# Optimization experiments

Measured on AMD Instinct MI355X. Metric: run time of the kernel, lower is better.

Reference implementation:

```python
import jax, jax.numpy as jnp
import numpy as np

N, E, B, H = 20000, 100000, 512, 64
IN_CH, EDGE_DIM, OUT_CH = 16, 8, 1


def setup_inputs() -> dict:
    key = jax.random.key(0)
    ks = jax.random.split(key, 20)
    rn = lambda k, shp, s=0.1: (jax.random.normal(k, shp, jnp.float32) * s)
    return {
        'x': rn(ks[0], (N, IN_CH), 1.0),
        'edge_index': jax.random.randint(ks[1], (2, E), 0, N),
        'edge_attr': rn(ks[2], (E, EDGE_DIM), 1.0),
        'batch': jnp.sort(jax.random.randint(ks[3], (N,), 0, B)),
        'lin0_w': rn(ks[4], (IN_CH, H)), 'lin0_b': jnp.zeros((H,), jnp.float32),
        'nn1_w': rn(ks[5], (EDGE_DIM, 128)), 'nn1_b': jnp.zeros((128,), jnp.float32),
        'nn2_w': rn(ks[6], (128, H * H), 0.02), 'nn2_b': jnp.zeros((H * H,), jnp.float32),
        'root_w': rn(ks[7], (H, H)), 'root_b': jnp.zeros((H,), jnp.float32),
        'gru_wih': rn(ks[8], (H, 3 * H)), 'gru_whh': rn(ks[9], (H, 3 * H)),
        'gru_bih': jnp.zeros((3 * H,), jnp.float32), 'gru_bhh': jnp.zeros((3 * H,), jnp.float32),
        'lstm_wih': rn(ks[10], (2 * H, 4 * H)), 'lstm_whh': rn(ks[11], (H, 4 * H)),
        'lstm_bih': jnp.zeros((4 * H,), jnp.float32), 'lstm_bhh': jnp.zeros((4 * H,), jnp.float32),
        'lin1_w': rn(ks[12], (2 * H, H)), 'lin1_b': jnp.zeros((H,), jnp.float32),
        'lin2_w': rn(ks[13], (H, OUT_CH)), 'lin2_b': jnp.zeros((OUT_CH,), jnp.float32),
    }


def reference(x, edge_index, edge_attr, batch, lin0_w, lin0_b, nn1_w, nn1_b,
              nn2_w, nn2_b, root_w, root_b, gru_wih, gru_whh, gru_bih, gru_bhh,
              lstm_wih, lstm_whh, lstm_bih, lstm_bhh, lin1_w, lin1_b, lin2_w, lin2_b):
    src, dst = edge_index[0], edge_index[1]
    # edge network weights (shared across the 3 message-passing steps)
    ew = jax.nn.relu(edge_attr @ nn1_w + nn1_b) @ nn2_w + nn2_b  # [E, H*H]
    ew = ew.reshape(E, H, H)
    deg = jnp.maximum(jax.ops.segment_sum(jnp.ones((E,), x.dtype), dst, N), 1.0)

    out = jax.nn.relu(x @ lin0_w + lin0_b)  # [N, H]
    h = out
    for _ in range(3):
        # NNConv: gather src feats, per-edge matvec, scatter-mean to dst, + root linear
        msg = jnp.einsum('ei,eio->eo', out[src], ew)                  # [E, H]
        agg = jax.ops.segment_sum(msg, dst, N) / deg[:, None]          # [N, H]
        m = jax.nn.relu(agg + out @ root_w + root_b)
        # GRU cell (torch gate order r, z, n)
        gi = m @ gru_wih + gru_bih
        gh = h @ gru_whh + gru_bhh
        r = jax.nn.sigmoid(gi[:, :H] + gh[:, :H])
        z = jax.nn.sigmoid(gi[:, H:2 * H] + gh[:, H:2 * H])
        n = jnp.tanh(gi[:, 2 * H:] + r * gh[:, 2 * H:])
        h = (1.0 - z) * n + z * h
        out = h

    # Set2Set pooling, 3 processing steps (torch LSTM gate order i, f, g, o)
    q_star = jnp.zeros((B, 2 * H), x.dtype)
    hh = jnp.zeros((B, H), x.dtype)
    cc = jnp.zeros((B, H), x.dtype)
    for _ in range(3):
        g = q_star @ lstm_wih + hh @ lstm_whh + lstm_bih + lstm_bhh    # [B, 4H]
        i_g = jax.nn.sigmoid(g[:, :H])
        f_g = jax.nn.sigmoid(g[:, H:2 * H])
        g_g = jnp.tanh(g[:, 2 * H:3 * H])
        o_g = jax.nn.sigmoid(g[:, 3 * H:])
        cc = f_g * cc + i_g * g_g
        hh = o_g * jnp.tanh(cc)
        q = hh                                                          # [B, H]
        e = jnp.sum(out * q[batch], axis=-1)                            # [N]
        e_max = jax.ops.segment_max(e, batch, B)
        a = jnp.exp(e - e_max[batch])
        a = a / jax.ops.segment_sum(a, batch, B)[batch]
        rvec = jax.ops.segment_sum(a[:, None] * out, batch, B)          # [B, H]
        q_star = jnp.concatenate([q, rvec], axis=-1)

    y = jax.nn.relu(q_star @ lin1_w + lin1_b) @ lin2_w + lin2_b         # [B, 1]
    return y
```

## Files before the change

### kernel.cpp

```cpp
#include <hip/hip_runtime.h>
#include <hip/hip_bf16.h>
#include <hip/hip_fp16.h>
#include <cstddef>
#include <cstdint>

#define N_NODES 20000
#define N_EDGES 100000
#define N_BATCH 512

typedef __attribute__((ext_vector_type(8))) short ushort8_t;
typedef __attribute__((ext_vector_type(8))) _Float16 f16x8;
typedef __attribute__((ext_vector_type(4))) float f32x4;

union F16x8U { f16x8 v; unsigned int u[4]; };

__device__ __forceinline__ float sigmoidf_(float x) { return 1.f / (1.f + expf(-x)); }
__device__ __forceinline__ unsigned short f2h(float x) {
    return __half_as_ushort(__float2half(x));
}

#define HB_BLOCKS 50000
#define LIN0_BLOCKS 5000
#define BSW_BLOCKS 258
#define DEG_BLOCKS 391

__global__ __launch_bounds__(256) void prep_kernel(
        const float* __restrict__ ea, const float* __restrict__ w1, const float* __restrict__ b1,
        const float* __restrict__ x, const float* __restrict__ l0w, const float* __restrict__ l0b,
        const float* __restrict__ w2, const float* __restrict__ b2,
        const int* __restrict__ ei,
        unsigned short* __restrict__ hb, float* __restrict__ out,
        unsigned short* __restrict__ bsw, float* __restrict__ deg, int E) {
    int bid = blockIdx.x, tid = threadIdx.x;
    if (bid < HB_BLOCKS) {
        int idx = bid * 256 + tid;
        int e = idx >> 7, j = idx & 127;
        float acc = b1[j];
#pragma unroll
        for (int i = 0; i < 8; i++) acc += ea[e * 8 + i] * w1[i * 128 + j];
        hb[idx] = f2h(fmaxf(acc, 0.f));
    } else if (bid < HB_BLOCKS + LIN0_BLOCKS) {
        int idx = (bid - HB_BLOCKS) * 256 + tid;
        int n = idx >> 6, j = idx & 63;
        float acc = l0b[j];
#pragma unroll
        for (int i = 0; i < 16; i++) acc += x[n * 16 + i] * l0w[i * 64 + j];
        out[idx] = fmaxf(acc, 0.f);
    } else if (bid < HB_BLOCKS + LIN0_BLOCKS + BSW_BLOCKS) {
        int idx = (bid - HB_BLOCKS - LIN0_BLOCKS) * 256 + tid;
        if (idx < 66048) {
            int l = idx & 63, oc = (idx >> 6) & 3, ks = idx >> 8;
            int o = oc * 16 + (l & 15);
            int kap0 = ks * 32 + 8 * (l >> 4);
#pragma unroll
            for (int j = 0; j < 8; ++j) {
                int kap = kap0 + j;
                int k = kap >> 6, i = kap & 63;
                float v = (k < 128) ? w2[(size_t)k * 4096 + i * 64 + o] : b2[i * 64 + o];
                bsw[(size_t)idx * 8 + j] = f2h(v);
            }
        }
    } else {
        int e = (bid - HB_BLOCKS - LIN0_BLOCKS - BSW_BLOCKS) * 256 + tid;
        if (e < E) atomicAdd(&deg[ei[E + e]], 1.0f);
    }
}

__global__ __launch_bounds__(256) void msg_mfma(const float* __restrict__ out,
                                                const unsigned short* __restrict__ hb,
                                                const unsigned short* __restrict__ bsw,
                                                const int* __restrict__ ei,
                                                float* __restrict__ agg, int E) {
    __shared__ __align__(16) unsigned int hs[129 * 64];
    const int tid = threadIdx.x;
    const int w = tid >> 6, l = tid & 63;
    const int e0 = blockIdx.x * 64;
    const int r16 = l & 15, q = l >> 4;

    {
        int e = e0 + l;
        bool v = e < E;
        const ushort8_t* hrow = (const ushort8_t*)(hb + (size_t)e * 128);
#pragma unroll
        for (int cc = 0; cc < 4; ++cc) {
            int c = w * 4 + cc;
            ushort8_t hv = {};
            if (v) hv = hrow[c];
#pragma unroll
            for (int j = 0; j < 8; ++j) {
                unsigned int hu = (unsigned short)hv[j];
                hs[(c * 8 + j) * 64 + l] = (hu << 16) | hu;
            }
        }
        if (w == 0) hs[128 * 64 + l] = v ? 0x3C003C00u : 0u;
    }

    f16x8 sfrag[4][2];
#pragma unroll
    for (int t = 0; t < 4; ++t) {
        int e = e0 + t * 16 + r16;
        int src = (e < E) ? ei[e] : 0;
        const f32x4* p = (const f32x4*)(out + (size_t)src * 64);
#pragma unroll
        for (int st = 0; st < 2; ++st) {
            f16x8 f = {};
            if (e < E) {
                f32x4 a = p[st * 8 + q * 2], b = p[st * 8 + q * 2 + 1];
#pragma unroll
                for (int j = 0; j < 4; ++j) { f[j] = (_Float16)a[j]; f[4 + j] = (_Float16)b[j]; }
            }
            sfrag[t][st] = f;
        }
    }

    const f16x8* bp = (const f16x8*)bsw;
    f16x8 bfA[8], bfB[8];
#pragma unroll
    for (int i = 0; i < 8; ++i) bfA[i] = bp[((w * 8 + i) << 6) + l];

    __syncthreads();

    f32x4 acc[4][4] = {};

#define MSG_COMPUTE(K, BF)                                                     \
    {                                                                          \
        _Pragma("unroll")                                                      \
        for (int t = 0; t < 4; ++t) {                                          \
            unsigned int hh = hs[(K) * 64 + t * 16 + r16];                     \
            _Pragma("unroll")                                                  \
            for (int st = 0; st < 2; ++st) {                                   \
                F16x8U s_, a_;                                                 \
                s_.v = sfrag[t][st];                                           \
                asm("v_pk_mul_f16 %0, %1, %2" : "=v"(a_.u[0]) : "v"(hh), "v"(s_.u[0])); \
                asm("v_pk_mul_f16 %0, %1, %2" : "=v"(a_.u[1]) : "v"(hh), "v"(s_.u[1])); \
                asm("v_pk_mul_f16 %0, %1, %2" : "=v"(a_.u[2]) : "v"(hh), "v"(s_.u[2])); \
                asm("v_pk_mul_f16 %0, %1, %2" : "=v"(a_.u[3]) : "v"(hh), "v"(s_.u[3])); \
                _Pragma("unroll")                                              \
                for (int oc = 0; oc < 4; ++oc)                                 \
                    acc[t][oc] = __builtin_amdgcn_mfma_f32_16x16x32_f16(       \
                        a_.v, BF[st * 4 + oc], acc[t][oc], 0, 0, 0);           \
            }                                                                  \
        }                                                                      \
    }

#pragma unroll 1
    for (int kk = 0; kk < 16; ++kk) {
        int k1 = w + kk * 8;
        int k2 = k1 + 4;
#pragma unroll
        for (int i = 0; i < 8; ++i) bfB[i] = bp[((k2 * 8 + i) << 6) + l];
        MSG_COMPUTE(k1, bfA);
        if (kk < 15) {
            int k3 = k1 + 8;
#pragma unroll
            for (int i = 0; i < 8; ++i) bfA[i] = bp[((k3 * 8 + i) << 6) + l];
        }
        MSG_COMPUTE(k2, bfB);
    }
#undef MSG_COMPUTE

    if (w == 0) {
#pragma unroll
        for (int i = 0; i < 8; ++i) bfA[i] = bp[((128 * 8 + i) << 6) + l];
#pragma unroll
        for (int t = 0; t < 4; ++t)
#pragma unroll
            for (int st = 0; st < 2; ++st)
#pragma unroll
                for (int oc = 0; oc < 4; ++oc)
                    acc[t][oc] = __builtin_amdgcn_mfma_f32_16x16x32_f16(
                        sfrag[t][st], bfA[st * 4 + oc], acc[t][oc], 0, 0, 0);
    }

#pragma unroll
    for (int t = 0; t < 4; ++t) {
#pragma unroll
        for (int r = 0; r < 4; ++r) {
            int e = e0 + t * 16 + q * 4 + r;
            if (e < E) {
                int dst = ei[E + e];
                float* arow = agg + (size_t)dst * 64 + r16;
#pragma unroll
                for (int oc = 0; oc < 4; ++oc)
                    atomicAdd(arow + oc * 16, acc[t][oc][r]);
            }
        }
    }
}

__global__ __launch_bounds__(256) void gru_kernel(float* __restrict__ out,
                                                  float* __restrict__ agg,
                                                  const float* __restrict__ deg,
                                                  const float* __restrict__ root_w,
                                                  const float* __restrict__ root_b,
                                                  const float* __restrict__ wih,
                                                  const float* __restrict__ whh,
                                                  const float* __restrict__ bih,
                                                  const float* __restrict__ bhh) {
    int w = threadIdx.x >> 6, j = threadIdx.x & 63;
    int n = blockIdx.x * 4 + w;
    __shared__ float s_o[4][64];
    __shared__ float s_m[4][64];
    s_o[w][j] = out[(size_t)n * 64 + j];
    __syncthreads();
    float d = deg[n]; if (d < 1.f) d = 1.f;
    float mv = agg[(size_t)n * 64 + j] / d + root_b[j];
    agg[(size_t)n * 64 + j] = 0.f;
#pragma unroll 8
    for (int i = 0; i < 64; i++) mv += s_o[w][i] * root_w[i * 64 + j];
    mv = fmaxf(mv, 0.f);
    s_m[w][j] = mv;
    __syncthreads();
    float gi_r = bih[j], gi_z = bih[64 + j], gi_n = bih[128 + j];
    float gh_r = bhh[j], gh_z = bhh[64 + j], gh_n = bhh[128 + j];
#pragma unroll 4
    for (int i = 0; i < 64; i++) {
        float m = s_m[w][i], hv = s_o[w][i];
        gi_r += m * wih[i * 192 + j];
        gi_z += m * wih[i * 192 + 64 + j];
        gi_n += m * wih[i * 192 + 128 + j];
        gh_r += hv * whh[i * 192 + j];
        gh_z += hv * whh[i * 192 + 64 + j];
        gh_n += hv * whh[i * 192 + 128 + j];
    }
    float r = sigmoidf_(gi_r + gh_r);
    float z = sigmoidf_(gi_z + gh_z);
    float nn = tanhf(gi_n + r * gh_n);
    float hnew = (1.f - z) * nn + z * s_o[w][j];
    out[(size_t)n * 64 + j] = hnew;
}

__global__ __launch_bounds__(256) void s2s_final(const float* __restrict__ out,
                                                 const int* __restrict__ batch,
                                                 const float* __restrict__ wih,
                                                 const float* __restrict__ whh,
                                                 const float* __restrict__ bih,
                                                 const float* __restrict__ bhh,
                                                 const float* __restrict__ w1,
                                                 const float* __restrict__ b1,
                                                 const float* __restrict__ w2,
                                                 const float* __restrict__ b2,
                                                 float* __restrict__ y, int N) {
    int b = blockIdx.x;
    int tid = threadIdx.x;
    int gate = tid >> 6, j = tid & 63;
    __shared__ float s_qs[128];
    __shared__ float s_g[4][64];
    __shared__ float s_h[64];
    __shared__ float s_c[64];
    __shared__ int s_lo, s_hi;
    __shared__ float s_red[4];
    __shared__ float s_rv[4][64];

    if (tid < 128) s_qs[tid] = 0.f;
    if (gate == 2) s_h[j] = 0.f;
    if (gate == 3) s_c[j] = 0.f;
    if (tid == 0) {
        int lo = 0, hi = N;
        while (lo < hi) { int mid = (lo + hi) >> 1; if (batch[mid] < b) lo = mid + 1; else hi = mid; }
        s_lo = lo;
        int lo2 = lo, hi2 = N;
        while (lo2 < hi2) { int mid = (lo2 + hi2) >> 1; if (batch[mid] < b + 1) lo2 = mid + 1; else hi2 = mid; }
        s_hi = lo2;
    }
    __syncthreads();

    for (int it = 0; it < 3; ++it) {
        float g = bih[gate * 64 + j] + bhh[gate * 64 + j];
#pragma unroll 4
        for (int i = 0; i < 128; ++i) g += s_qs[i] * wih[i * 256 + gate * 64 + j];
#pragma unroll 4
        for (int i = 0; i < 64; ++i) g += s_h[i] * whh[i * 256 + gate * 64 + j];
        s_g[gate][j] = g;
        __syncthreads();
        if (gate == 0) {
            float c = sigmoidf_(s_g[1][j]) * s_c[j] + sigmoidf_(s_g[0][j]) * tanhf(s_g[2][j]);
            float h = sigmoidf_(s_g[3][j]) * tanhf(c);
            s_c[j] = c;
            s_h[j] = h;
            s_qs[j] = h;
        }
        __syncthreads();

        int lo = s_lo, hi = s_hi;
        float wmax = -3.402823e38f;
        for (int n = lo + gate; n < hi; n += 4) {
            float p = out[(size_t)n * 64 + j] * s_h[j];
#pragma unroll
            for (int d = 32; d >= 1; d >>= 1) p += __shfl_xor(p, d);
            wmax = fmaxf(wmax, p);
        }
        if (j == 0) s_red[gate] = wmax;
        __syncthreads();
        float m = fmaxf(fmaxf(s_red[0], s_red[1]), fmaxf(s_red[2], s_red[3]));
        __syncthreads();
        float ssum = 0.f, rv = 0.f;
        for (int n = lo + gate; n < hi; n += 4) {
            float xv = out[(size_t)n * 64 + j];
            float p = xv * s_h[j];
#pragma unroll
            for (int d = 32; d >= 1; d >>= 1) p += __shfl_xor(p, d);
            float a = expf(p - m);
            ssum += a;
            rv += a * xv;
        }
        if (j == 0) s_red[gate] = ssum;
        s_rv[gate][j] = rv;
        __syncthreads();
        if (gate == 0) {
            float S = s_red[0] + s_red[1] + s_red[2] + s_red[3];
            float r = s_rv[0][j] + s_rv[1][j] + s_rv[2][j] + s_rv[3][j];
            s_qs[64 + j] = (S > 0.f) ? r / S : 0.f;
        }
        __syncthreads();
    }

    if (gate == 0) {
        float tv = b1[j];
#pragma unroll 4
        for (int i = 0; i < 128; ++i) tv += s_qs[i] * w1[i * 64 + j];
        tv = fmaxf(tv, 0.f);
        float p = tv * w2[j];
#pragma unroll
        for (int d = 32; d >= 1; d >>= 1) p += __shfl_xor(p, d);
        if (j == 0) y[b] = p + b2[0];
    }
}

extern "C" void kernel_launch(void* const* d_in, const int* in_sizes, int n_in,
                              void* d_out, int out_size, void* d_ws, size_t ws_size,
                              hipStream_t stream) {
    const int N = N_NODES, E = N_EDGES, B = N_BATCH;
    const float* x       = (const float*)d_in[0];
    const int*   ei      = (const int*)d_in[1];
    const float* ea      = (const float*)d_in[2];
    const int*   batch   = (const int*)d_in[3];
    const float* lin0_w  = (const float*)d_in[4];
    const float* lin0_b  = (const float*)d_in[5];
    const float* nn1_w   = (const float*)d_in[6];
    const float* nn1_b   = (const float*)d_in[7];
    const float* nn2_w   = (const float*)d_in[8];
    const float* nn2_b   = (const float*)d_in[9];
    const float* root_w  = (const float*)d_in[10];
    const float* root_b  = (const float*)d_in[11];
    const float* gru_wih = (const float*)d_in[12];
    const float* gru_whh = (const float*)d_in[13];
    const float* gru_bih = (const float*)d_in[14];
    const float* gru_bhh = (const float*)d_in[15];
    const float* lstm_wih = (const float*)d_in[16];
    const float* lstm_whh = (const float*)d_in[17];
    const float* lstm_bih = (const float*)d_in[18];
    const float* lstm_bhh = (const float*)d_in[19];
    const float* lin1_w  = (const float*)d_in[20];
    const float* lin1_b  = (const float*)d_in[21];
    const float* lin2_w  = (const float*)d_in[22];
    const float* lin2_b  = (const float*)d_in[23];
    float* y = (float*)d_out;

    char* ws = (char*)d_ws;
    size_t off = 0;
    auto alloc = [&](size_t bytes) { void* p = ws + off; off = (off + bytes + 255) & ~(size_t)255; return p; };
    unsigned short* hb  = (unsigned short*)alloc((size_t)E * 128 * 2);
    unsigned short* bsw = (unsigned short*)alloc((size_t)66048 * 8 * 2);
    float* out   = (float*)alloc((size_t)N * 64 * 4);
    float* agg   = (float*)alloc((size_t)N * 64 * 4);
    float* deg   = (float*)alloc((size_t)N * 4);

    hipMemsetAsync(deg, 0, (size_t)N * 4, stream);
    hipMemsetAsync(agg, 0, (size_t)N * 64 * 4, stream);

    prep_kernel<<<HB_BLOCKS + LIN0_BLOCKS + BSW_BLOCKS + DEG_BLOCKS, 256, 0, stream>>>(
        ea, nn1_w, nn1_b, x, lin0_w, lin0_b, nn2_w, nn2_b, ei, hb, out, bsw, deg, E);

    for (int step = 0; step < 3; ++step) {
        msg_mfma<<<(E + 63) / 64, 256, 0, stream>>>(out, hb, bsw, ei, agg, E);
        gru_kernel<<<N / 4, 256, 0, stream>>>(out, agg, deg, root_w, root_b,
                                              gru_wih, gru_whh, gru_bih, gru_bhh);
    }

    s2s_final<<<B, 256, 0, stream>>>(out, batch, lstm_wih, lstm_whh, lstm_bih, lstm_bhh,
                                     lin1_w, lin1_b, lin2_w, lin2_b, y, N);
}
```

Baseline: 823.8 us.

## Enlarge msg_mfma edge tile to 96 and store edge scalars as 16-bit in LDS

Each block now handles 96 edges (six 16-row MFMA tiles) instead of 64. Every streamed B fragment of the edge-network weight is therefore reused across more edges, cutting global weight traffic per edge. The LDS copy of the per-edge hidden values shrinks to 16-bit, and the multiply broadcasts the low half via op_sel_hi, which keeps shared memory usage small. This costs more accumulator and fragment registers and a launch-bounds hint of 2 blocks, which may cause spills. Only the first 96 threads now fill LDS, so that fill is less parallel.

```diff
diff --git a/kernel.cpp b/kernel.cpp
--- a/kernel.cpp
+++ b/kernel.cpp
@@ -7,6 +7,9 @@
 #define N_NODES 20000
 #define N_EDGES 100000
 #define N_BATCH 512
+
+#define EPB 96
+#define TS 6
 
 typedef __attribute__((ext_vector_type(8))) short ushort8_t;
 typedef __attribute__((ext_vector_type(8))) _Float16 f16x8;
@@ -66,38 +69,35 @@
     }
 }
 
-__global__ __launch_bounds__(256) void msg_mfma(const float* __restrict__ out,
-                                                const unsigned short* __restrict__ hb,
-                                                const unsigned short* __restrict__ bsw,
-                                                const int* __restrict__ ei,
-                                                float* __restrict__ agg, int E) {
-    __shared__ __align__(16) unsigned int hs[129 * 64];
+__global__ __launch_bounds__(256, 2) void msg_mfma(const float* __restrict__ out,
+                                                   const unsigned short* __restrict__ hb,
+                                                   const unsigned short* __restrict__ bsw,
+                                                   const int* __restrict__ ei,
+                                                   float* __restrict__ agg, int E) {
+    __shared__ __align__(16) unsigned short hs16[129 * EPB];
     const int tid = threadIdx.x;
     const int w = tid >> 6, l = tid & 63;
-    const int e0 = blockIdx.x * 64;
+    const int e0 = blockIdx.x * EPB;
     const int r16 = l & 15, q = l >> 4;
 
-    {
-        int e = e0 + l;
+    if (tid < EPB) {
+        int e = e0 + tid;
         bool v = e < E;
         const ushort8_t* hrow = (const ushort8_t*)(hb + (size_t)e * 128);
 #pragma unroll
-        for (int cc = 0; cc < 4; ++cc) {
-            int c = w * 4 + cc;
+        for (int c = 0; c < 16; ++c) {
             ushort8_t hv = {};
             if (v) hv = hrow[c];
 #pragma unroll
-            for (int j = 0; j < 8; ++j) {
-                unsigned int hu = (unsigned short)hv[j];
-                hs[(c * 8 + j) * 64 + l] = (hu << 16) | hu;
-            }
-        }
-        if (w == 0) hs[128 * 64 + l] = v ? 0x3C003C00u : 0u;
-    }
-
-    f16x8 sfrag[4][2];
-#pragma unroll
-    for (int t = 0; t < 4; ++t) {
+            for (int j = 0; j < 8; ++j)
+                hs16[(c * 8 + j) * EPB + tid] = (unsigned short)hv[j];
+        }
+        hs16[128 * EPB + tid] = v ? (unsigned short)0x3C00 : (unsigned short)0;
+    }
+
+    f16x8 sfrag[TS][2];
+#pragma unroll
+    for (int t = 0; t < TS; ++t) {
         int e = e0 + t * 16 + r16;
         int src = (e < E) ? ei[e] : 0;
         const f32x4* p = (const f32x4*)(out + (size_t)src * 64);
@@ -120,21 +120,25 @@
 
     __syncthreads();
 
-    f32x4 acc[4][4] = {};
+    f32x4 acc[TS][4] = {};
 
 #define MSG_COMPUTE(K, BF)                                                     \
     {                                                                          \
         _Pragma("unroll")                                                      \
-        for (int t = 0; t < 4; ++t) {                                          \
-            unsigned int hh = hs[(K) * 64 + t * 16 + r16];                     \
+        for (int t = 0; t < TS; ++t) {                                         \
+            unsigned int hu = hs16[(K) * EPB + t * 16 + r16];                  \
             _Pragma("unroll")                                                  \
             for (int st = 0; st < 2; ++st) {                                   \
                 F16x8U s_, a_;                                                 \
                 s_.v = sfrag[t][st];                                           \
-                asm("v_pk_mul_f16 %0, %1, %2" : "=v"(a_.u[0]) : "v"(hh), "v"(s_.u[0])); \
-                asm("v_pk_mul_f16 %0, %1, %2" : "=v"(a_.u[1]) : "v"(hh), "v"(s_.u[1])); \
-                asm("v_pk_mul_f16 %0, %1, %2" : "=v"(a_.u[2]) : "v"(hh), "v"(s_.u[2])); \
-                asm("v_pk_mul_f16 %0, %1, %2" : "=v"(a_.u[3]) : "v"(hh), "v"(s_.u[3])); \
+                asm("v_pk_mul_f16 %0, %1, %2 op_sel:[0,0] op_sel_hi:[0,1]"     \
+                    : "=v"(a_.u[0]) : "v"(hu), "v"(s_.u[0]));                  \
+                asm("v_pk_mul_f16 %0, %1, %2 op_sel:[0,0] op_sel_hi:[0,1]"     \
+                    : "=v"(a_.u[1]) : "v"(hu), "v"(s_.u[1]));                  \
+                asm("v_pk_mul_f16 %0, %1, %2 op_sel:[0,0] op_sel_hi:[0,1]"     \
+                    : "=v"(a_.u[2]) : "v"(hu), "v"(s_.u[2]));                  \
+                asm("v_pk_mul_f16 %0, %1, %2 op_sel:[0,0] op_sel_hi:[0,1]"     \
+                    : "=v"(a_.u[3]) : "v"(hu), "v"(s_.u[3]));                  \
                 _Pragma("unroll")                                              \
                 for (int oc = 0; oc < 4; ++oc)                                 \
                     acc[t][oc] = __builtin_amdgcn_mfma_f32_16x16x32_f16(       \
@@ -163,7 +167,7 @@
 #pragma unroll
         for (int i = 0; i < 8; ++i) bfA[i] = bp[((128 * 8 + i) << 6) + l];
 #pragma unroll
-        for (int t = 0; t < 4; ++t)
+        for (int t = 0; t < TS; ++t)
 #pragma unroll
             for (int st = 0; st < 2; ++st)
 #pragma unroll
@@ -173,7 +177,7 @@
     }
 
 #pragma unroll
-    for (int t = 0; t < 4; ++t) {
+    for (int t = 0; t < TS; ++t) {
 #pragma unroll
         for (int r = 0; r < 4; ++r) {
             int e = e0 + t * 16 + q * 4 + r;
@@ -373,7 +377,7 @@
         ea, nn1_w, nn1_b, x, lin0_w, lin0_b, nn2_w, nn2_b, ei, hb, out, bsw, deg, E);
 
     for (int step = 0; step < 3; ++step) {
-        msg_mfma<<<(E + 63) / 64, 256, 0, stream>>>(out, hb, bsw, ei, agg, E);
+        msg_mfma<<<(E + EPB - 1) / EPB, 256, 0, stream>>>(out, hb, bsw, ei, agg, E);
         gru_kernel<<<N / 4, 256, 0, stream>>>(out, agg, deg, root_w, root_b,
                                               gru_wih, gru_whh, gru_bih, gru_bhh);
     }
```

Measured after the change: 850.5 us. 1.03x slower.
